# Optimization experiments

Measured on AMD Instinct MI355X. Metric: run time of the kernel, lower is better.

Reference implementation:

```python
import jax, jax.numpy as jnp
import numpy as np

D_MODEL = 768
NUM_HEADS = 12
D_K = D_MODEL // NUM_HEADS
B, S = 2, 4096


def setup_inputs() -> dict:
    key = jax.random.key(0)
    ks = jax.random.split(key, 11)
    std = 1.0 / np.sqrt(D_MODEL)
    mk = lambda k: (jax.random.normal(k, (D_MODEL, D_MODEL), jnp.float32) * std)
    return {
        "query": jax.random.normal(ks[0], (B, S, D_MODEL), jnp.float32),
        "key": jax.random.normal(ks[1], (B, S, D_MODEL), jnp.float32),
        "value": jax.random.normal(ks[2], (B, S, D_MODEL), jnp.float32),
        "Wq": mk(ks[3]), "bq": jnp.zeros((D_MODEL,), jnp.float32),
        "Wk": mk(ks[4]), "bk": jnp.zeros((D_MODEL,), jnp.float32),
        "Wv": mk(ks[5]), "bv": jnp.zeros((D_MODEL,), jnp.float32),
        "Wo": mk(ks[6]), "bo": jnp.zeros((D_MODEL,), jnp.float32),
    }


def _split_heads(x):
    # [B,S,D] -> [B,H,S,d_k]
    b, s, _ = x.shape
    return x.reshape(b, s, NUM_HEADS, D_K).transpose(0, 2, 1, 3)


def reference(query, key, value, Wq, bq, Wk, bk, Wv, bv, Wo, bo):
    q = _split_heads(query @ Wq.T + bq)
    k = _split_heads(key @ Wk.T + bk)
    v = _split_heads(value @ Wv.T + bv)
    scores = jnp.einsum("bhqd,bhkd->bhqk", q, k) / jnp.sqrt(jnp.float32(D_K))
    attn = jax.nn.softmax(scores, axis=-1)  # dropout is identity in eval
    out = jnp.einsum("bhqk,bhkd->bhqd", attn, v)
    out = out.transpose(0, 2, 1, 3).reshape(query.shape[0], -1, D_MODEL)
    return out @ Wo.T + bo
```

## Files before the change

### kernel.cpp

```cpp
#include <hip/hip_runtime.h>
#include <cstdint>

#define D_MODEL 768
#define NHEAD 12
#define DK 64
#define BATCH 2
#define SEQ 4096
#define MTOT (BATCH * SEQ)
#define NT (SEQ / 64)
#define WSZ (D_MODEL * D_MODEL)

typedef __attribute__((ext_vector_type(8))) _Float16 f16x8;
typedef __attribute__((ext_vector_type(2))) _Float16 f16x2;
typedef __attribute__((ext_vector_type(4))) float f32x4;
typedef unsigned short ushort_t;
typedef unsigned int uint_t;

#define SCALE_LOG2E 0.18033688011112042f
#define EXP2(d, s) asm("v_exp_f32 %0, %1" : "=v"(d) : "v"(s))

__device__ __forceinline__ int swz(int row, int col_e) {
    return (row * 128 + col_e * 2) ^ ((row & 7) << 4);
}

__device__ __forceinline__ uint_t pkrtz(float a, float b) {
    return __builtin_bit_cast(uint_t, __builtin_amdgcn_cvt_pkrtz(a, b));
}

__global__ __launch_bounds__(256) void cvt7(const float* s0, const float* s1, const float* s2,
                                            const float* s3, const float* s4, const float* s5,
                                            const float* s6, ushort_t* d0, ushort_t* d1,
                                            ushort_t* d2, ushort_t* d3, ushort_t* d4,
                                            ushort_t* d5, ushort_t* d6) {
    const int t = blockIdx.y;
    const float* src;
    ushort_t* dst;
    int n;
    if (t == 0) { src = s0; dst = d0; n = MTOT * D_MODEL; }
    else if (t == 1) { src = s1; dst = d1; n = MTOT * D_MODEL; }
    else if (t == 2) { src = s2; dst = d2; n = MTOT * D_MODEL; }
    else if (t == 3) { src = s3; dst = d3; n = WSZ; }
    else if (t == 4) { src = s4; dst = d4; n = WSZ; }
    else if (t == 5) { src = s5; dst = d5; n = WSZ; }
    else { src = s6; dst = d6; n = WSZ; }
    const int i = (blockIdx.x * 256 + threadIdx.x) * 8;
    if (i >= n) return;
    float4 a = *(const float4*)(src + i);
    float4 b = *(const float4*)(src + i + 4);
    f16x8 h;
    h[0] = (_Float16)a.x; h[1] = (_Float16)a.y; h[2] = (_Float16)a.z; h[3] = (_Float16)a.w;
    h[4] = (_Float16)b.x; h[5] = (_Float16)b.y; h[6] = (_Float16)b.z; h[7] = (_Float16)b.w;
    *(f16x8*)(dst + i) = h;
}

template <int MODE>
__global__ __launch_bounds__(256) void gemm_f16(const ushort_t* __restrict__ Ap,
                                                const ushort_t* __restrict__ Wp,
                                                const float* __restrict__ bias,
                                                void* __restrict__ Cp,
                                                float alpha) {
    __shared__ __align__(16) char lds[24576];
    const int tid = threadIdx.x;
    const int lane = tid & 63;
    const int w = tid >> 6;
    const int li = lane & 15;
    const int g = lane >> 4;
    const int wr = w >> 1, wc = w & 1;
    const int m0 = blockIdx.y * 128;
    const int n0 = blockIdx.x * 64;

    f32x4 acc[4][2];
#pragma unroll
    for (int fr = 0; fr < 4; ++fr)
#pragma unroll
        for (int fc = 0; fc < 2; ++fc) acc[fr][fc] = (f32x4){0.f, 0.f, 0.f, 0.f};

    for (int k0 = 0; k0 < D_MODEL; k0 += 64) {
        __syncthreads();
#pragma unroll
        for (int i = 0; i < 4; ++i) {
            const int c = tid + i * 256;
            const int row = c >> 3;
            const int c8 = (c & 7) * 8;
            *(f16x8*)(lds + swz(row, c8)) =
                *(const f16x8*)(Ap + (size_t)(m0 + row) * D_MODEL + k0 + c8);
        }
#pragma unroll
        for (int i = 0; i < 2; ++i) {
            const int c = tid + i * 256;
            const int row = c >> 3;
            const int c8 = (c & 7) * 8;
            *(f16x8*)(lds + 16384 + swz(row, c8)) =
                *(const f16x8*)(Wp + (size_t)(n0 + row) * D_MODEL + k0 + c8);
        }
        __syncthreads();
#pragma unroll
        for (int ks = 0; ks < 2; ++ks) {
            f16x8 ar[4], br[2];
#pragma unroll
            for (int fr = 0; fr < 4; ++fr)
                ar[fr] = *(const f16x8*)(lds + swz(wr * 64 + fr * 16 + li, ks * 32 + g * 8));
#pragma unroll
            for (int fc = 0; fc < 2; ++fc)
                br[fc] = *(const f16x8*)(lds + 16384 + swz(wc * 32 + fc * 16 + li, ks * 32 + g * 8));
#pragma unroll
            for (int fr = 0; fr < 4; ++fr)
#pragma unroll
                for (int fc = 0; fc < 2; ++fc)
                    acc[fr][fc] = __builtin_amdgcn_mfma_f32_16x16x32_f16(ar[fr], br[fc], acc[fr][fc], 0, 0, 0);
        }
    }

#pragma unroll
    for (int fr = 0; fr < 4; ++fr)
#pragma unroll
        for (int fc = 0; fc < 2; ++fc)
#pragma unroll
            for (int r = 0; r < 4; ++r) {
                const int m = m0 + wr * 64 + fr * 16 + g * 4 + r;
                const int d = wc * 32 + fc * 16 + li;
                float val = acc[fr][fc][r] + bias[n0 + d];
                if (MODE == 0) {
                    ((float*)Cp)[(size_t)m * D_MODEL + n0 + d] = val;
                } else {
                    val *= alpha;
                    const int b = m >> 12;
                    const int s = m & (SEQ - 1);
                    const size_t idx = (((size_t)b * NHEAD + blockIdx.x) * SEQ + s) * DK + d;
                    ((ushort_t*)Cp)[idx] = __builtin_bit_cast(ushort_t, (_Float16)val);
                }
            }
}

__global__ __launch_bounds__(256, 4) void flash4(const ushort_t* __restrict__ q_g,
                                                 const ushort_t* __restrict__ k_g,
                                                 const ushort_t* __restrict__ v_g,
                                                 ushort_t* __restrict__ aw) {
    __shared__ __align__(16) char lds[40960];

    const int tid = threadIdx.x;
    const int lane = tid & 63;
    const int w = tid >> 6;
    const int li = lane & 15;
    const int g = lane >> 4;
    const int bh = blockIdx.y;
    const int q0 = blockIdx.x * 64;

    const ushort_t* qp = q_g + (size_t)bh * SEQ * DK;
    const ushort_t* kp = k_g + (size_t)bh * SEQ * DK;
    const ushort_t* vp = v_g + (size_t)bh * SEQ * DK;

    f16x8 qf[2];
#pragma unroll
    for (int ks = 0; ks < 2; ++ks)
        qf[ks] = *(const f16x8*)(qp + (size_t)(q0 + w * 16 + li) * DK + ks * 32 + g * 8);

    const int srow = tid >> 2;
    const int sc0 = (tid & 3) * 16;
    const int kwr0 = swz(srow, sc0);
    const int kwr1 = swz(srow, sc0 + 8);
    const int vd = lane;

    f16x8 kpre[2][2];
    ushort4 vpre[2][4];
    {
        const ushort_t* ks_ = kp + (size_t)srow * DK + sc0;
        kpre[0][0] = *(const f16x8*)ks_;
        kpre[0][1] = *(const f16x8*)(ks_ + 8);
        const ushort_t* vs_ = vp + (size_t)(w * 16) * DK + vd;
#pragma unroll
        for (int j4 = 0; j4 < 4; ++j4) {
            vpre[0][j4].x = vs_[(j4 * 4 + 0) * DK];
            vpre[0][j4].y = vs_[(j4 * 4 + 1) * DK];
            vpre[0][j4].z = vs_[(j4 * 4 + 2) * DK];
            vpre[0][j4].w = vs_[(j4 * 4 + 3) * DK];
        }
    }

    f32x4 oacc[4];
#pragma unroll
    for (int i = 0; i < 4; ++i) oacc[i] = (f32x4){0.f, 0.f, 0.f, 0.f};
    float m_r = -1e30f, l_r = 0.f;

    const int pb = 32768 + w * 2048;

    for (int kt2 = 0; kt2 < NT / 2; ++kt2) {
#pragma unroll
        for (int ph = 0; ph < 2; ++ph) {
            const int kt = kt2 * 2 + ph;
            const int KB = ph ? 8192 : 0;
            const int VB = ph ? 24576 : 16384;

            *(f16x8*)(lds + KB + kwr0) = kpre[ph][0];
            *(f16x8*)(lds + KB + kwr1) = kpre[ph][1];
#pragma unroll
            for (int j4 = 0; j4 < 4; ++j4)
                *(ushort4*)(lds + VB + swz(vd, w * 16 + j4 * 4)) = vpre[ph][j4];
            __syncthreads();

            if (kt + 1 < NT) {
                const ushort_t* ks_ = kp + (size_t)((kt + 1) * 64 + srow) * DK + sc0;
                kpre[ph ^ 1][0] = *(const f16x8*)ks_;
                kpre[ph ^ 1][1] = *(const f16x8*)(ks_ + 8);
                const ushort_t* vs_ = vp + (size_t)((kt + 1) * 64 + w * 16) * DK + vd;
#pragma unroll
                for (int j4 = 0; j4 < 4; ++j4) {
                    vpre[ph ^ 1][j4].x = vs_[(j4 * 4 + 0) * DK];
                    vpre[ph ^ 1][j4].y = vs_[(j4 * 4 + 1) * DK];
                    vpre[ph ^ 1][j4].z = vs_[(j4 * 4 + 2) * DK];
                    vpre[ph ^ 1][j4].w = vs_[(j4 * 4 + 3) * DK];
                }
            }

            f32x4 sacc[4];
#pragma unroll
            for (int t = 0; t < 4; ++t) {
                sacc[t] = (f32x4){0.f, 0.f, 0.f, 0.f};
#pragma unroll
                for (int ks = 0; ks < 2; ++ks) {
                    f16x8 kf = *(const f16x8*)(lds + KB + swz(t * 16 + li, ks * 32 + g * 8));
                    sacc[t] = __builtin_amdgcn_mfma_f32_16x16x32_f16(kf, qf[ks], sacc[t], 0, 0, 0);
                }
            }

            float t0 = fmaxf(fmaxf(sacc[0][0], sacc[0][1]), fmaxf(sacc[0][2], sacc[0][3]));
            float t1 = fmaxf(fmaxf(sacc[1][0], sacc[1][1]), fmaxf(sacc[1][2], sacc[1][3]));
            float t2 = fmaxf(fmaxf(sacc[2][0], sacc[2][1]), fmaxf(sacc[2][2], sacc[2][3]));
            float t3 = fmaxf(fmaxf(sacc[3][0], sacc[3][1]), fmaxf(sacc[3][2], sacc[3][3]));
            float mx = fmaxf(fmaxf(t0, t1), fmaxf(t2, t3));
            mx = fmaxf(mx, __shfl_xor(mx, 16));
            mx = fmaxf(mx, __shfl_xor(mx, 32));

            if (__any(mx > m_r + 8.0f)) {
                const float nm = fmaxf(m_r, mx);
                float corr;
                float dd = m_r - nm;
                EXP2(corr, dd);
                m_r = nm;
                l_r *= corr;
#pragma unroll
                for (int dt = 0; dt < 4; ++dt) oacc[dt] *= corr;
            }

#pragma unroll
            for (int t = 0; t < 4; ++t) {
                float p0, p1, p2, p3;
                float e0 = sacc[t][0] - m_r;
                float e1 = sacc[t][1] - m_r;
                float e2 = sacc[t][2] - m_r;
                float e3 = sacc[t][3] - m_r;
                EXP2(p0, e0); EXP2(p1, e1); EXP2(p2, e2); EXP2(p3, e3);
                l_r += (p0 + p1) + (p2 + p3);
                uint2 pk;
                pk.x = pkrtz(p0, p1);
                pk.y = pkrtz(p2, p3);
                *(uint2*)(lds + pb + swz(li, t * 16 + g * 4)) = pk;
            }

            f16x8 pbf[2];
#pragma unroll
            for (int ks = 0; ks < 2; ++ks)
                pbf[ks] = *(const f16x8*)(lds + pb + swz(li, ks * 32 + g * 8));
#pragma unroll
            for (int dt = 0; dt < 4; ++dt)
#pragma unroll
                for (int ks = 0; ks < 2; ++ks) {
                    f16x8 vf = *(const f16x8*)(lds + VB + swz(dt * 16 + li, ks * 32 + g * 8));
                    oacc[dt] = __builtin_amdgcn_mfma_f32_16x16x32_f16(vf, pbf[ks], oacc[dt], 0, 0, 0);
                }
        }
    }

    float lt = l_r;
    lt += __shfl_xor(lt, 16);
    lt += __shfl_xor(lt, 32);
    const float inv = 1.0f / lt;
    const int b = bh / NHEAD;
    const int hh = bh % NHEAD;
    const int qrow = q0 + w * 16 + li;
#pragma unroll
    for (int dt = 0; dt < 4; ++dt) {
        uint2 o;
        o.x = pkrtz(oacc[dt][0] * inv, oacc[dt][1] * inv);
        o.y = pkrtz(oacc[dt][2] * inv, oacc[dt][3] * inv);
        *(uint2*)&aw[((size_t)b * SEQ + qrow) * D_MODEL + hh * DK + dt * 16 + g * 4] = o;
    }
}

extern "C" void kernel_launch(void* const* d_in, const int* in_sizes, int n_in,
                              void* d_out, int out_size, void* d_ws, size_t ws_size,
                              hipStream_t stream) {
    const float* q_in = (const float*)d_in[0];
    const float* k_in = (const float*)d_in[1];
    const float* v_in = (const float*)d_in[2];
    const float* Wq = (const float*)d_in[3];
    const float* bq = (const float*)d_in[4];
    const float* Wk = (const float*)d_in[5];
    const float* bk = (const float*)d_in[6];
    const float* Wv = (const float*)d_in[7];
    const float* bv = (const float*)d_in[8];
    const float* Wo = (const float*)d_in[9];
    const float* bo = (const float*)d_in[10];
    float* out = (float*)d_out;

    const size_t per = (size_t)MTOT * D_MODEL;
    ushort_t* x16q = (ushort_t*)d_ws;
    ushort_t* x16k = x16q + per;
    ushort_t* x16v = x16k + per;
    ushort_t* w16 = x16v + per;
    ushort_t* qh = w16 + 4 * (size_t)WSZ;
    ushort_t* kh = qh + per;
    ushort_t* vh = kh + per;
    ushort_t* aw = vh + per;

    dim3 blk(256);
    dim3 gcvt(MTOT * D_MODEL / (256 * 8), 7);
    hipLaunchKernelGGL(cvt7, gcvt, blk, 0, stream, q_in, k_in, v_in, Wq, Wk, Wv, Wo,
                       x16q, x16k, x16v, w16, w16 + WSZ, w16 + 2 * WSZ, w16 + 3 * WSZ);

    dim3 gproj(D_MODEL / 64, MTOT / 128);
    hipLaunchKernelGGL((gemm_f16<1>), gproj, blk, 0, stream, x16q, w16, bq, qh, SCALE_LOG2E);
    hipLaunchKernelGGL((gemm_f16<1>), gproj, blk, 0, stream, x16k, w16 + WSZ, bk, kh, 1.0f);
    hipLaunchKernelGGL((gemm_f16<1>), gproj, blk, 0, stream, x16v, w16 + 2 * WSZ, bv, vh, 1.0f);

    dim3 gattn(SEQ / 64, BATCH * NHEAD);
    hipLaunchKernelGGL(flash4, gattn, blk, 0, stream, qh, kh, vh, aw);

    hipLaunchKernelGGL((gemm_f16<0>), gproj, blk, 0, stream, aw, w16 + 3 * WSZ, bo, out, 1.0f);
}
```

Before: 411.5 us.

## Use direct global-to-LDS loads with double buffering in GEMM and 512-thread attention

The projection GEMM now stages A and W tiles with global_load_lds straight into swizzled LDS and double-buffers across k-steps, so the next tile loads while the current one is computed and only one barrier is needed per step. The flash kernel grows to 512 threads covering 128 query rows, which halves the number of K/V tile loads per query. It loads K via global_load_lds and prefetches V into registers, writing V to LDS after the PV MFMAs. This is meant to cut register staging and barrier stalls, at the cost of more LDS per block (which may lower occupancy) and tighter ordering requirements around the asynchronous LDS writes.

```diff
diff --git a/kernel.cpp b/kernel.cpp
--- a/kernel.cpp
+++ b/kernel.cpp
@@ -11,7 +11,6 @@
 #define WSZ (D_MODEL * D_MODEL)
 
 typedef __attribute__((ext_vector_type(8))) _Float16 f16x8;
-typedef __attribute__((ext_vector_type(2))) _Float16 f16x2;
 typedef __attribute__((ext_vector_type(4))) float f32x4;
 typedef unsigned short ushort_t;
 typedef unsigned int uint_t;
@@ -25,6 +24,11 @@
 
 __device__ __forceinline__ uint_t pkrtz(float a, float b) {
     return __builtin_bit_cast(uint_t, __builtin_amdgcn_cvt_pkrtz(a, b));
+}
+
+__device__ __forceinline__ void gl_lds16(const ushort_t* g, char* l) {
+    __builtin_amdgcn_global_load_lds((const __attribute__((address_space(1))) void*)g,
+                                     (__attribute__((address_space(3))) void*)l, 16, 0, 0);
 }
 
 __global__ __launch_bounds__(256) void cvt7(const float* s0, const float* s1, const float* s2,
@@ -53,13 +57,29 @@
     *(f16x8*)(dst + i) = h;
 }
 
+__device__ __forceinline__ void stage_gemm(const ushort_t* __restrict__ Ap,
+                                           const ushort_t* __restrict__ Wp,
+                                           int m0, int n0, int k0, char* ldsbuf,
+                                           int w, int lane) {
+    const int r8 = lane >> 3;
+    const int cole = (((lane & 7) * 16) ^ (r8 << 4)) >> 1;
+#pragma unroll
+    for (int j = 0; j < 4; ++j)
+        gl_lds16(Ap + (size_t)(m0 + w * 32 + j * 8 + r8) * D_MODEL + k0 + cole,
+                 ldsbuf + w * 4096 + j * 1024);
+#pragma unroll
+    for (int j = 0; j < 2; ++j)
+        gl_lds16(Wp + (size_t)(n0 + w * 16 + j * 8 + r8) * D_MODEL + k0 + cole,
+                 ldsbuf + 16384 + w * 2048 + j * 1024);
+}
+
 template <int MODE>
 __global__ __launch_bounds__(256) void gemm_f16(const ushort_t* __restrict__ Ap,
                                                 const ushort_t* __restrict__ Wp,
                                                 const float* __restrict__ bias,
                                                 void* __restrict__ Cp,
                                                 float alpha) {
-    __shared__ __align__(16) char lds[24576];
+    __shared__ __align__(16) char lds[49152];
     const int tid = threadIdx.x;
     const int lane = tid & 63;
     const int w = tid >> 6;
@@ -75,39 +95,32 @@
 #pragma unroll
         for (int fc = 0; fc < 2; ++fc) acc[fr][fc] = (f32x4){0.f, 0.f, 0.f, 0.f};
 
-    for (int k0 = 0; k0 < D_MODEL; k0 += 64) {
-        __syncthreads();
-#pragma unroll
-        for (int i = 0; i < 4; ++i) {
-            const int c = tid + i * 256;
-            const int row = c >> 3;
-            const int c8 = (c & 7) * 8;
-            *(f16x8*)(lds + swz(row, c8)) =
-                *(const f16x8*)(Ap + (size_t)(m0 + row) * D_MODEL + k0 + c8);
-        }
-#pragma unroll
-        for (int i = 0; i < 2; ++i) {
-            const int c = tid + i * 256;
-            const int row = c >> 3;
-            const int c8 = (c & 7) * 8;
-            *(f16x8*)(lds + 16384 + swz(row, c8)) =
-                *(const f16x8*)(Wp + (size_t)(n0 + row) * D_MODEL + k0 + c8);
-        }
-        __syncthreads();
-#pragma unroll
-        for (int ks = 0; ks < 2; ++ks) {
-            f16x8 ar[4], br[2];
-#pragma unroll
-            for (int fr = 0; fr < 4; ++fr)
-                ar[fr] = *(const f16x8*)(lds + swz(wr * 64 + fr * 16 + li, ks * 32 + g * 8));
-#pragma unroll
-            for (int fc = 0; fc < 2; ++fc)
-                br[fc] = *(const f16x8*)(lds + 16384 + swz(wc * 32 + fc * 16 + li, ks * 32 + g * 8));
-#pragma unroll
-            for (int fr = 0; fr < 4; ++fr)
+    stage_gemm(Ap, Wp, m0, n0, 0, lds, w, lane);
+    __syncthreads();
+
+    for (int kk = 0; kk < 6; ++kk) {
+#pragma unroll
+        for (int ph = 0; ph < 2; ++ph) {
+            const int it = kk * 2 + ph;
+            char* cur = lds + (ph ? 24576 : 0);
+            if (it + 1 < 12)
+                stage_gemm(Ap, Wp, m0, n0, (it + 1) * 64, lds + (ph ? 0 : 24576), w, lane);
+#pragma unroll
+            for (int ks = 0; ks < 2; ++ks) {
+                f16x8 ar[4], br[2];
+#pragma unroll
+                for (int fr = 0; fr < 4; ++fr)
+                    ar[fr] = *(const f16x8*)(cur + swz(wr * 64 + fr * 16 + li, ks * 32 + g * 8));
 #pragma unroll
                 for (int fc = 0; fc < 2; ++fc)
-                    acc[fr][fc] = __builtin_amdgcn_mfma_f32_16x16x32_f16(ar[fr], br[fc], acc[fr][fc], 0, 0, 0);
+                    br[fc] = *(const f16x8*)(cur + 16384 + swz(wc * 32 + fc * 16 + li, ks * 32 + g * 8));
+#pragma unroll
+                for (int fr = 0; fr < 4; ++fr)
+#pragma unroll
+                    for (int fc = 0; fc < 2; ++fc)
+                        acc[fr][fc] = __builtin_amdgcn_mfma_f32_16x16x32_f16(ar[fr], br[fc], acc[fr][fc], 0, 0, 0);
+            }
+            if (it + 1 < 12) __syncthreads();
         }
     }
 
@@ -132,11 +145,11 @@
             }
 }
 
-__global__ __launch_bounds__(256, 4) void flash4(const ushort_t* __restrict__ q_g,
+__global__ __launch_bounds__(512, 4) void flash5(const ushort_t* __restrict__ q_g,
                                                  const ushort_t* __restrict__ k_g,
                                                  const ushort_t* __restrict__ v_g,
                                                  ushort_t* __restrict__ aw) {
-    __shared__ __align__(16) char lds[40960];
+    __shared__ __align__(16) char lds[49152];
 
     const int tid = threadIdx.x;
     const int lane = tid & 63;
@@ -144,7 +157,7 @@
     const int li = lane & 15;
     const int g = lane >> 4;
     const int bh = blockIdx.y;
-    const int q0 = blockIdx.x * 64;
+    const int q0 = blockIdx.x * 128;
 
     const ushort_t* qp = q_g + (size_t)bh * SEQ * DK;
     const ushort_t* kp = k_g + (size_t)bh * SEQ * DK;
@@ -155,27 +168,29 @@
     for (int ks = 0; ks < 2; ++ks)
         qf[ks] = *(const f16x8*)(qp + (size_t)(q0 + w * 16 + li) * DK + ks * 32 + g * 8);
 
-    const int srow = tid >> 2;
-    const int sc0 = (tid & 3) * 16;
-    const int kwr0 = swz(srow, sc0);
-    const int kwr1 = swz(srow, sc0 + 8);
+    const int kr8 = lane >> 3;
+    const int kcole = (((lane & 7) * 16) ^ (kr8 << 4)) >> 1;
+    const ushort_t* ksrc = kp + (size_t)(w * 8 + kr8) * DK + kcole;
+    char* const kdst0 = lds + 0 + w * 1024;
+    char* const kdst1 = lds + 8192 + w * 1024;
+
     const int vd = lane;
-
-    f16x8 kpre[2][2];
-    ushort4 vpre[2][4];
+    const ushort_t* vsrc = vp + (size_t)(w * 8) * DK + vd;
+    const int vw0 = swz(vd, w * 8);
+    const int vw1 = swz(vd, w * 8 + 4);
+
+    gl_lds16(ksrc, kdst0);
+    ushort_t vr[8];
+#pragma unroll
+    for (int j = 0; j < 8; ++j) vr[j] = vsrc[(size_t)j * DK];
     {
-        const ushort_t* ks_ = kp + (size_t)srow * DK + sc0;
-        kpre[0][0] = *(const f16x8*)ks_;
-        kpre[0][1] = *(const f16x8*)(ks_ + 8);
-        const ushort_t* vs_ = vp + (size_t)(w * 16) * DK + vd;
-#pragma unroll
-        for (int j4 = 0; j4 < 4; ++j4) {
-            vpre[0][j4].x = vs_[(j4 * 4 + 0) * DK];
-            vpre[0][j4].y = vs_[(j4 * 4 + 1) * DK];
-            vpre[0][j4].z = vs_[(j4 * 4 + 2) * DK];
-            vpre[0][j4].w = vs_[(j4 * 4 + 3) * DK];
-        }
+        ushort4 u0, u1;
+        u0.x = vr[0]; u0.y = vr[1]; u0.z = vr[2]; u0.w = vr[3];
+        u1.x = vr[4]; u1.y = vr[5]; u1.z = vr[6]; u1.w = vr[7];
+        *(ushort4*)(lds + 16384 + vw0) = u0;
+        *(ushort4*)(lds + 16384 + vw1) = u1;
     }
+    __syncthreads();
 
     f32x4 oacc[4];
 #pragma unroll
@@ -188,28 +203,16 @@
 #pragma unroll
         for (int ph = 0; ph < 2; ++ph) {
             const int kt = kt2 * 2 + ph;
-            const int KB = ph ? 8192 : 0;
-            const int VB = ph ? 24576 : 16384;
-
-            *(f16x8*)(lds + KB + kwr0) = kpre[ph][0];
-            *(f16x8*)(lds + KB + kwr1) = kpre[ph][1];
-#pragma unroll
-            for (int j4 = 0; j4 < 4; ++j4)
-                *(ushort4*)(lds + VB + swz(vd, w * 16 + j4 * 4)) = vpre[ph][j4];
-            __syncthreads();
-
-            if (kt + 1 < NT) {
-                const ushort_t* ks_ = kp + (size_t)((kt + 1) * 64 + srow) * DK + sc0;
-                kpre[ph ^ 1][0] = *(const f16x8*)ks_;
-                kpre[ph ^ 1][1] = *(const f16x8*)(ks_ + 8);
-                const ushort_t* vs_ = vp + (size_t)((kt + 1) * 64 + w * 16) * DK + vd;
-#pragma unroll
-                for (int j4 = 0; j4 < 4; ++j4) {
-                    vpre[ph ^ 1][j4].x = vs_[(j4 * 4 + 0) * DK];
-                    vpre[ph ^ 1][j4].y = vs_[(j4 * 4 + 1) * DK];
-                    vpre[ph ^ 1][j4].z = vs_[(j4 * 4 + 2) * DK];
-                    vpre[ph ^ 1][j4].w = vs_[(j4 * 4 + 3) * DK];
-                }
+            const int KBc = ph ? 8192 : 0;
+            const int VBc = ph ? 24576 : 16384;
+            const int VBn = ph ? 16384 : 24576;
+            const bool pre = (kt + 1 < NT);
+
+            if (pre) {
+                gl_lds16(ksrc + (size_t)(kt + 1) * 64 * DK, ph ? kdst0 : kdst1);
+#pragma unroll
+                for (int j = 0; j < 8; ++j)
+                    vr[j] = vsrc[((size_t)(kt + 1) * 64 + j) * DK];
             }
 
             f32x4 sacc[4];
@@ -218,7 +221,7 @@
                 sacc[t] = (f32x4){0.f, 0.f, 0.f, 0.f};
 #pragma unroll
                 for (int ks = 0; ks < 2; ++ks) {
-                    f16x8 kf = *(const f16x8*)(lds + KB + swz(t * 16 + li, ks * 32 + g * 8));
+                    f16x8 kf = *(const f16x8*)(lds + KBc + swz(t * 16 + li, ks * 32 + g * 8));
                     sacc[t] = __builtin_amdgcn_mfma_f32_16x16x32_f16(kf, qf[ks], sacc[t], 0, 0, 0);
                 }
             }
@@ -265,9 +268,18 @@
             for (int dt = 0; dt < 4; ++dt)
 #pragma unroll
                 for (int ks = 0; ks < 2; ++ks) {
-                    f16x8 vf = *(const f16x8*)(lds + VB + swz(dt * 16 + li, ks * 32 + g * 8));
+                    f16x8 vf = *(const f16x8*)(lds + VBc + swz(dt * 16 + li, ks * 32 + g * 8));
                     oacc[dt] = __builtin_amdgcn_mfma_f32_16x16x32_f16(vf, pbf[ks], oacc[dt], 0, 0, 0);
                 }
+
+            if (pre) {
+                ushort4 u0, u1;
+                u0.x = vr[0]; u0.y = vr[1]; u0.z = vr[2]; u0.w = vr[3];
+                u1.x = vr[4]; u1.y = vr[5]; u1.z = vr[6]; u1.w = vr[7];
+                *(ushort4*)(lds + VBn + vw0) = u0;
+                *(ushort4*)(lds + VBn + vw1) = u1;
+                __syncthreads();
+            }
         }
     }
 
@@ -323,8 +335,8 @@
     hipLaunchKernelGGL((gemm_f16<1>), gproj, blk, 0, stream, x16k, w16 + WSZ, bk, kh, 1.0f);
     hipLaunchKernelGGL((gemm_f16<1>), gproj, blk, 0, stream, x16v, w16 + 2 * WSZ, bv, vh, 1.0f);
 
-    dim3 gattn(SEQ / 64, BATCH * NHEAD);
-    hipLaunchKernelGGL(flash4, gattn, blk, 0, stream, qh, kh, vh, aw);
+    dim3 gattn(SEQ / 128, BATCH * NHEAD);
+    hipLaunchKernelGGL(flash5, gattn, dim3(512), 0, stream, qh, kh, vh, aw);
 
     hipLaunchKernelGGL((gemm_f16<0>), gproj, blk, 0, stream, aw, w16 + 3 * WSZ, bo, out, 1.0f);
 }
```

New measurement: 374.6 us. -9.0%, faster.
